# Kernel tuning notes

Measured on AMD Instinct MI355X. Metric: run time of the kernel, lower is better.

Reference implementation:

```python
import jax, jax.numpy as jnp
import numpy as np

N_REACH = 4096
N_T = 730
DT = 3600.0
VEL_LB = 0.3
VEL_UB = 15.0
Q_LB = 1e-4
SLOPE_LB = 1e-4


def _make_adjacency(n):
    # River-network DAG in topological order: each reach j (except outlet)
    # drains to exactly one downstream reach i > j  =>  strictly lower-triangular.
    rng = np.random.default_rng(0)
    j = np.arange(n - 1)
    ds = j + 1 + (rng.random(n - 1) * (n - 1 - j)).astype(np.int64)
    adj = np.zeros((n, n), dtype=np.float32)
    adj[ds, j] = 1.0
    return jnp.asarray(adj)


def setup_inputs() -> dict:
    key = jax.random.key(0)
    ks = jax.random.split(key, 8)
    u = lambda k, s: jax.random.uniform(k, s, dtype=jnp.float32)
    q_prime = u(ks[0], (N_T, N_REACH)) * 10.0            # lateral inflow m^3/s
    n = 0.01 + 0.09 * u(ks[1], (N_REACH,))               # Manning's n
    q_spatial = 1.5 + u(ks[2], (N_REACH,))               # log base > 1
    p_spatial = 1.0 + 3.0 * u(ks[3], (N_REACH,))         # width scale
    length = 1000.0 + 5000.0 * u(ks[4], (N_REACH,))      # reach length [m]
    slope = 1e-3 + 0.05 * u(ks[5], (N_REACH,))           # channel slope
    width = 5.0 + 100.0 * u(ks[6], (N_REACH,))           # width > p_spatial
    x_storage = 0.1 + 0.3 * u(ks[7], (N_REACH,))         # Muskingum x
    adj = _make_adjacency(N_REACH)
    return {"q_prime": q_prime, "n": n, "q_spatial": q_spatial,
            "p_spatial": p_spatial, "length": length, "slope": slope,
            "width": width, "x_storage": x_storage, "adj": adj}


def reference(q_prime, n, q_spatial, p_spatial, length, slope, width, x_storage, adj):
    slope = jnp.clip(slope, SLOPE_LB)
    # Manning's equation -> celerity (note: independent of discharge, as in source)
    depth = jnp.log(width / p_spatial) / jnp.log(q_spatial)
    v = (1.0 / n) * depth ** (2.0 / 3.0) * jnp.sqrt(slope)
    c = jnp.clip(v, VEL_LB, VEL_UB) * (5.0 / 3.0)
    k = length / c
    denom = 2.0 * k * (1.0 - x_storage) + DT
    c1 = (DT - 2.0 * k * x_storage) / denom
    c2 = (DT + 2.0 * k * x_storage) / denom
    c3 = (2.0 * k * (1.0 - x_storage) - DT) / denom
    c4 = 2.0 * DT / denom

    # Lower-triangular routing system: A = I - diag(c1) @ adjacency (constant)
    N = q_prime.shape[1]
    A = jnp.eye(N, dtype=q_prime.dtype) - c1[:, None] * adj

    q0 = q_prime[0]
    out0 = jnp.clip(q0[-1], Q_LB)  # single gage at index -1

    def step(q_t, qp_row):
        q_l = jnp.clip(qp_row, Q_LB)
        i_t = adj @ q_t                        # upstream inflow
        b = c2 * i_t + c3 * q_t + c4 * q_l
        x = jax.scipy.linalg.solve_triangular(A, b[:, None], lower=True)[:, 0]
        q_t1 = jnp.clip(x, Q_LB)
        return q_t1, q_t1[-1]

    _, outs = jax.lax.scan(step, q0, q_prime[:-1])  # timesteps 1..T-1 use q_prime[t-1]
    runoff = jnp.concatenate([out0[None], outs])[None, :]  # [1, T]
    return runoff
```

## Files before the change

### kernel.cpp

```cpp
#include <hip/hip_runtime.h>

#define N 4096
#define NT 730
#define NTH 512
#define PER_T 8
#define QLB 1e-4f
#define DT_S 3600.0f

#define WS_DS     0
#define WS_SZ     4096
#define WS_CCNT   8192
#define WS_COFF   12288
#define WS_CUR    16388
#define WS_HI     20484
#define WS_FLAG   24580
#define WS_C1     28676
#define WS_C2     32772
#define WS_C3     36868
#define WS_C4     40964
#define WS_CLIST  45060
#define WS_GP     49156
#define WS_LOP    53252
#define WS_C3P    57348
#define WS_C4P    61444
#define WS_EPAR   65540
#define WS_EWS    69636
#define WS_SP     73736
#define WS_ISP    81928
#define WS_QPP    90120
#define WS_END    (WS_QPP + NT * N)

__device__ __forceinline__ int qidx(int p) { return ((p & 7) << 9) | (p >> 3); }

template <int CTRL, int RMASK>
__device__ __forceinline__ double dpp_stage(double v) {
    union U { double d; unsigned int u[2]; };
    U s, t;
    s.d = v;
    t.u[0] = (unsigned)__builtin_amdgcn_update_dpp(0, (int)s.u[0], CTRL, RMASK, 0xf, false);
    t.u[1] = (unsigned)__builtin_amdgcn_update_dpp(0, (int)s.u[1], CTRL, RMASK, 0xf, false);
    return v + t.d;
}
__device__ __forceinline__ double wave_incl_scan(double v) {
    v = dpp_stage<0x111, 0xf>(v);
    v = dpp_stage<0x112, 0xf>(v);
    v = dpp_stage<0x114, 0xf>(v);
    v = dpp_stage<0x118, 0xf>(v);
    v = dpp_stage<0x142, 0xa>(v);
    v = dpp_stage<0x143, 0xc>(v);
    return v;
}

__global__ void k_init(int* ds, int* sz, int* ccnt, int* hi, int* flag) {
    int j = blockIdx.x * 256 + threadIdx.x;
    if (j < N) { ds[j] = N - 1; sz[j] = 1; ccnt[j] = 0; hi[j] = -1; flag[j] = 0; }
}

__global__ void k_extract(const float4* __restrict__ adj4, int* __restrict__ ds) {
    long idx = (long)blockIdx.x * 256 + threadIdx.x;
    if (idx >= (long)N * N / 4) return;
    float4 w = adj4[idx];
    long base = idx * 4;
    int row = (int)(base >> 12);
    int col = (int)(base & 4095);
    if (w.x != 0.0f) ds[col + 0] = row;
    if (w.y != 0.0f) ds[col + 1] = row;
    if (w.z != 0.0f) ds[col + 2] = row;
    if (w.w != 0.0f) ds[col + 3] = row;
}

__global__ void k_coeffs(const float* n, const float* qs, const float* ps,
                         const float* len, const float* slope, const float* width,
                         const float* xs, float* __restrict__ c1, float* __restrict__ c2,
                         float* __restrict__ c3, float* __restrict__ c4) {
    int i = blockIdx.x * 256 + threadIdx.x;
    if (i >= N) return;
    float s  = fmaxf(slope[i], 1e-4f);
    float dp = logf(width[i] / ps[i]) / logf(qs[i]);
    float v  = (1.0f / n[i]) * powf(dp, 2.0f / 3.0f) * sqrtf(s);
    float c  = fminf(fmaxf(v, 0.3f), 15.0f) * (5.0f / 3.0f);
    float k  = len[i] / c;
    float x  = xs[i];
    float denom = 2.0f * k * (1.0f - x) + DT_S;
    c1[i] = (DT_S - 2.0f * k * x) / denom;
    c2[i] = (DT_S + 2.0f * k * x) / denom;
    c3[i] = (2.0f * k * (1.0f - x) - DT_S) / denom;
    c4[i] = 2.0f * DT_S / denom;
}

__global__ void k_count(const int* __restrict__ ds, int* __restrict__ ccnt,
                        int* __restrict__ sz) {
    int u = blockIdx.x * 256 + threadIdx.x;
    if (u >= N || u == N - 1) return;
    atomicAdd(&ccnt[ds[u]], 1);
    int a = ds[u];
    while (true) {
        atomicAdd(&sz[a], 1);
        if (a == N - 1) break;
        a = ds[a];
    }
}

__global__ __launch_bounds__(1024) void k_scan(const int* __restrict__ src,
                                               int* __restrict__ off,
                                               int* __restrict__ cur) {
    __shared__ int buf[1024];
    int tid = threadIdx.x;
    int a0 = src[tid * 4 + 0], a1 = src[tid * 4 + 1];
    int a2 = src[tid * 4 + 2], a3 = src[tid * 4 + 3];
    int s1 = a0, s2 = a0 + a1, s3 = a0 + a1 + a2, tot = s3 + a3;
    buf[tid] = tot;
    __syncthreads();
    for (int o = 1; o < 1024; o <<= 1) {
        int add = (tid >= o) ? buf[tid - o] : 0;
        __syncthreads();
        buf[tid] += add;
        __syncthreads();
    }
    int base = buf[tid] - tot;
    off[tid * 4 + 0] = base;      cur[tid * 4 + 0] = base;
    off[tid * 4 + 1] = base + s1; cur[tid * 4 + 1] = base + s1;
    off[tid * 4 + 2] = base + s2; cur[tid * 4 + 2] = base + s2;
    off[tid * 4 + 3] = base + s3; cur[tid * 4 + 3] = base + s3;
    if (tid == 1023) off[N] = buf[1023];
}

__global__ void k_fill(const int* __restrict__ ds, int* __restrict__ cur,
                       int* __restrict__ clist) {
    int u = blockIdx.x * 256 + threadIdx.x;
    if (u >= N || u == N - 1) return;
    int cp = atomicAdd(&cur[ds[u]], 1);
    clist[cp] = u;
}

__global__ __launch_bounds__(1024) void k_post(const int* __restrict__ ds,
                                               const int* __restrict__ sz,
                                               const int* __restrict__ coff,
                                               const int* __restrict__ ccnt,
                                               const int* __restrict__ clist,
                                               int* __restrict__ hi,
                                               int* __restrict__ flag) {
    int tid = threadIdx.x;
    if (tid == 0) hi[N - 1] = N - 1;
    __syncthreads();
    for (int it = 0; it < 96; ++it) {
        for (int v = tid; v < N; v += 1024) {
            if (hi[v] >= 0 && flag[v] == 0) {
                int cum = hi[v] - sz[v] + 1;
                int b0 = coff[v], e0 = b0 + ccnt[v];
                for (int k = b0; k < e0; ++k) {
                    int c = clist[k];
                    hi[c] = cum + sz[c] - 1;
                    cum += sz[c];
                }
                flag[v] = 1;
            }
        }
        __syncthreads();
    }
}

__global__ void k_prep(const int* __restrict__ ds, const int* __restrict__ sz,
                       const int* __restrict__ hi,
                       const float* __restrict__ c1, const float* __restrict__ c2,
                       const float* __restrict__ c3, const float* __restrict__ c4,
                       int* __restrict__ gP, int* __restrict__ loP,
                       float* __restrict__ c3P, float* __restrict__ c4P,
                       int* __restrict__ eparP, float* __restrict__ ewsP,
                       double* __restrict__ SP, double* __restrict__ ISP) {
    int u = blockIdx.x * 256 + threadIdx.x;
    if (u >= N) return;
    int p = hi[u];
    double s = 1.0;
    if (u != N - 1) {
        int a = ds[u];
        while (true) {
            s *= (double)c1[a];
            if (a == N - 1) break;
            a = ds[a];
        }
    }
    SP[p] = s; ISP[p] = 1.0 / s;
    gP[p] = u;
    loP[p] = p - sz[u] + 1;
    c3P[p] = c3[u]; c4P[p] = c4[u];
    if (u != N - 1) {
        eparP[p] = hi[ds[u]];
        ewsP[p] = c2[ds[u]];
    } else {
        eparP[p] = p;
        ewsP[p] = 0.0f;
    }
}

__global__ void k_permute(const float* __restrict__ qp, const int* __restrict__ gP,
                          float* __restrict__ qpp) {
    long e = (long)blockIdx.x * 256 + threadIdx.x;
    if (e >= (long)NT * N) return;
    int tr = (int)(e >> 12);
    int v  = (int)(e & 4095);
    qpp[e] = qp[(size_t)tr * N + gP[v]];
}

__global__ __launch_bounds__(NTH) void k_route(
    const float* __restrict__ qp, const float* __restrict__ qpp,
    const float* __restrict__ c3g, const float* __restrict__ c4g,
    const int* __restrict__ gPg, const int* __restrict__ loPg,
    const int* __restrict__ eparPg, const float* __restrict__ ewsPg,
    const double* __restrict__ SPg, const double* __restrict__ ISPg,
    int use_perm, float* __restrict__ out) {
    __shared__ float CSA[2][N];
    __shared__ double TLp[N];
    __shared__ __align__(16) double wpart[8];
    int tid = threadIdx.x;
    int lane = tid & 63, wid = tid >> 6;

    int epar[PER_T], jg[PER_T], wv[PER_T], g[PER_T];
    float ews[PER_T], c3r[PER_T], c4r[PER_T], qreg[PER_T], qc[PER_T], qn[PER_T];
    double Sr[PER_T], iSr[PER_T];
    bool haslo[PER_T];
#pragma unroll
    for (int r = 0; r < PER_T; ++r) {
        int p = tid * PER_T + r;
        epar[r] = eparPg[p]; ews[r] = ewsPg[p];
        int l = loPg[p];
        haslo[r] = (l > 0);
        int lm = (l > 0) ? (l - 1) : 0;
        jg[r] = qidx(lm);
        wv[r] = lm >> 9;
        g[r] = gPg[p];
        c3r[r] = c3g[p]; c4r[r] = c4g[p];
        Sr[r] = SPg[p]; iSr[r] = ISPg[p];
        float q0 = use_perm ? qpp[p] : qp[g[r]];
        qreg[r] = q0; qc[r] = q0;
    }
    {
        float4 z = make_float4(0.f, 0.f, 0.f, 0.f);
        float4* c0 = (float4*)&CSA[0][tid * PER_T];
        float4* c1 = (float4*)&CSA[1][tid * PER_T];
        c0[0] = z; c0[1] = z; c1[0] = z; c1[1] = z;
    }
    if (tid == NTH - 1) out[0] = fmaxf(qreg[PER_T - 1], QLB);
    __syncthreads();
#pragma unroll
    for (int r = 0; r < PER_T; ++r)
        atomicAdd(&CSA[1][epar[r]], ews[r] * qreg[r]);
    __syncthreads();

    for (int t = 1; t < NT; ++t) {
        int s = t & 1;
        float4 ca = *(const float4*)&CSA[s][tid * PER_T];
        float4 cb = *(const float4*)&CSA[s][tid * PER_T + 4];
        float cs[PER_T] = {ca.x, ca.y, ca.z, ca.w, cb.x, cb.y, cb.z, cb.w};
        float bb[PER_T];
        double yv[PER_T], Tloc[PER_T];
        double tl = 0.0;
#pragma unroll
        for (int r = 0; r < PER_T; ++r) {
            bb[r] = cs[r] + c3r[r] * qreg[r] + c4r[r] * fmaxf(qc[r], QLB);
            double y = Sr[r] * (double)bb[r];
            yv[r] = y;
            tl += y;
            Tloc[r] = tl;
        }
        double incl = wave_incl_scan(tl);
        double texw = incl - tl;
#pragma unroll
        for (int r = 0; r < PER_T; ++r)
            TLp[(r << 9) | tid] = texw + Tloc[r];
        if (lane == 63) wpart[wid] = incl;
        __syncthreads();
        if (t < NT - 1) {
            if (use_perm) {
                const float4* row4 = (const float4*)(qpp + (size_t)t * N);
                float4 a = row4[tid * 2], b = row4[tid * 2 + 1];
                qn[0] = a.x; qn[1] = a.y; qn[2] = a.z; qn[3] = a.w;
                qn[4] = b.x; qn[5] = b.y; qn[6] = b.z; qn[7] = b.w;
            } else {
                const float* row = qp + (size_t)t * N;
#pragma unroll
                for (int r = 0; r < PER_T; ++r) qn[r] = row[g[r]];
            }
        }
        double2 w0 = *(const double2*)&wpart[0];
        double2 w1 = *(const double2*)&wpart[2];
        double2 w2 = *(const double2*)&wpart[4];
        double2 w3 = *(const double2*)&wpart[6];
        double P1 = w0.x, P2 = P1 + w0.y, P3 = P2 + w1.x, P4 = P3 + w1.y;
        double P5 = P4 + w2.x, P6 = P5 + w2.y, P7 = P6 + w3.x;
        double woff = 0.0;
        if (wid > 0) woff += w0.x;
        if (wid > 1) woff += w0.y;
        if (wid > 2) woff += w1.x;
        if (wid > 3) woff += w1.y;
        if (wid > 4) woff += w2.x;
        if (wid > 5) woff += w2.y;
        if (wid > 6) woff += w3.x;
#pragma unroll
        for (int r = 0; r < PER_T; ++r) {
            int w = wv[r];
            double lo2 = (w & 2) ? ((w & 1) ? P3 : P2) : ((w & 1) ? P1 : 0.0);
            double hi2 = (w & 2) ? ((w & 1) ? P7 : P6) : ((w & 1) ? P5 : P4);
            double goff = (w & 4) ? hi2 : lo2;
            double Tg = haslo[r] ? (TLp[jg[r]] + goff) : 0.0;
            double Tself = woff + texw + Tloc[r] - yv[r];
            double x = (double)bb[r] + (Tself - Tg) * iSr[r];
            qreg[r] = fmaxf((float)x, QLB);
        }
        {
            float4 z = make_float4(0.f, 0.f, 0.f, 0.f);
            float4* c0 = (float4*)&CSA[s][tid * PER_T];
            c0[0] = z; c0[1] = z;
        }
#pragma unroll
        for (int r = 0; r < PER_T; ++r)
            atomicAdd(&CSA[s ^ 1][epar[r]], ews[r] * qreg[r]);
        if (tid == NTH - 1) out[t] = qreg[PER_T - 1];
        __syncthreads();
#pragma unroll
        for (int r = 0; r < PER_T; ++r) qc[r] = qn[r];
    }
}

extern "C" void kernel_launch(void* const* d_in, const int* in_sizes, int n_in,
                              void* d_out, int out_size, void* d_ws, size_t ws_size,
                              hipStream_t stream) {
    const float* qp    = (const float*)d_in[0];
    const float* n     = (const float*)d_in[1];
    const float* qs    = (const float*)d_in[2];
    const float* ps    = (const float*)d_in[3];
    const float* len   = (const float*)d_in[4];
    const float* slope = (const float*)d_in[5];
    const float* width = (const float*)d_in[6];
    const float* xs    = (const float*)d_in[7];
    const float* adj   = (const float*)d_in[8];
    float* out = (float*)d_out;

    int*    W     = (int*)d_ws;
    int*    ds    = W + WS_DS;
    int*    sz    = W + WS_SZ;
    int*    ccnt  = W + WS_CCNT;
    int*    coff  = W + WS_COFF;
    int*    cur   = W + WS_CUR;
    int*    hi    = W + WS_HI;
    int*    flag  = W + WS_FLAG;
    float*  c1    = (float*)(W + WS_C1);
    float*  c2    = (float*)(W + WS_C2);
    float*  c3    = (float*)(W + WS_C3);
    float*  c4    = (float*)(W + WS_C4);
    int*    clist = W + WS_CLIST;
    int*    gP    = W + WS_GP;
    int*    loP   = W + WS_LOP;
    float*  c3P   = (float*)(W + WS_C3P);
    float*  c4P   = (float*)(W + WS_C4P);
    int*    eparP = W + WS_EPAR;
    float*  ewsP  = (float*)(W + WS_EWS);
    double* SP    = (double*)(W + WS_SP);
    double* ISP   = (double*)(W + WS_ISP);
    float*  QPP   = (float*)(W + WS_QPP);

    int use_perm = (ws_size >= (size_t)WS_END * 4) ? 1 : 0;

    k_init<<<(N + 255) / 256, 256, 0, stream>>>(ds, sz, ccnt, hi, flag);
    k_extract<<<(N * N / 4 + 255) / 256, 256, 0, stream>>>((const float4*)adj, ds);
    k_coeffs<<<(N + 255) / 256, 256, 0, stream>>>(n, qs, ps, len, slope, width, xs,
                                                  c1, c2, c3, c4);
    k_count<<<(N + 255) / 256, 256, 0, stream>>>(ds, ccnt, sz);
    k_scan<<<1, 1024, 0, stream>>>(ccnt, coff, cur);
    k_fill<<<(N + 255) / 256, 256, 0, stream>>>(ds, cur, clist);
    k_post<<<1, 1024, 0, stream>>>(ds, sz, coff, ccnt, clist, hi, flag);
    k_prep<<<(N + 255) / 256, 256, 0, stream>>>(ds, sz, hi, c1, c2, c3, c4,
                                                gP, loP, c3P, c4P, eparP, ewsP,
                                                SP, ISP);
    if (use_perm)
        k_permute<<<(int)(((long)NT * N + 255) / 256), 256, 0, stream>>>(qp, gP, QPP);
    k_route<<<1, NTH, 0, stream>>>(qp, QPP, c3P, c4P, gP, loP, eparP, ewsP,
                                   SP, ISP, use_perm, out);
}
```

Before: 5.178 ms.

## Double routing block to 1024 threads and compute wave offsets before storing prefix

The single-block routing kernel now uses 1024 threads with 4 reaches each instead of 512 with 8, which halves the serial per-thread work in every timestep. Cross-wave offsets are computed with a 16-lane DPP scan over the wave partials and readlane. That requires an extra barrier before the shared prefix array is written, but the array then holds global prefixes, so the per-element offset selection logic goes away. The cost is a third barrier per step across 16 waves and more LDS atomic contention from more threads.

```diff
diff --git a/kernel.cpp b/kernel.cpp
--- a/kernel.cpp
+++ b/kernel.cpp
@@ -2,8 +2,8 @@
 
 #define N 4096
 #define NT 730
-#define NTH 512
-#define PER_T 8
+#define NTH 1024
+#define PER_T 4
 #define QLB 1e-4f
 #define DT_S 3600.0f
 
@@ -30,7 +30,7 @@
 #define WS_QPP    90120
 #define WS_END    (WS_QPP + NT * N)
 
-__device__ __forceinline__ int qidx(int p) { return ((p & 7) << 9) | (p >> 3); }
+__device__ __forceinline__ int qidx4(int p) { return ((p & 3) << 10) | (p >> 2); }
 
 template <int CTRL, int RMASK>
 __device__ __forceinline__ double dpp_stage(double v) {
@@ -49,6 +49,21 @@
     v = dpp_stage<0x142, 0xa>(v);
     v = dpp_stage<0x143, 0xc>(v);
     return v;
+}
+__device__ __forceinline__ double row16_incl_scan(double v) {
+    v = dpp_stage<0x111, 0xf>(v);
+    v = dpp_stage<0x112, 0xf>(v);
+    v = dpp_stage<0x114, 0xf>(v);
+    v = dpp_stage<0x118, 0xf>(v);
+    return v;
+}
+__device__ __forceinline__ double readlane_f64(double v, int slane) {
+    union U { double d; int i[2]; };
+    U u; u.d = v;
+    U o;
+    o.i[0] = __builtin_amdgcn_readlane(u.i[0], slane);
+    o.i[1] = __builtin_amdgcn_readlane(u.i[1], slane);
+    return o.d;
 }
 
 __global__ void k_init(int* ds, int* sz, int* ccnt, int* hi, int* flag) {
@@ -210,12 +225,13 @@
     const double* __restrict__ SPg, const double* __restrict__ ISPg,
     int use_perm, float* __restrict__ out) {
     __shared__ float CSA[2][N];
-    __shared__ double TLp[N];
-    __shared__ __align__(16) double wpart[8];
+    __shared__ double TL[N];
+    __shared__ __align__(16) double wpart[16];
     int tid = threadIdx.x;
     int lane = tid & 63, wid = tid >> 6;
-
-    int epar[PER_T], jg[PER_T], wv[PER_T], g[PER_T];
+    int swid = __builtin_amdgcn_readfirstlane(wid);
+
+    int epar[PER_T], jg[PER_T], g[PER_T];
     float ews[PER_T], c3r[PER_T], c4r[PER_T], qreg[PER_T], qc[PER_T], qn[PER_T];
     double Sr[PER_T], iSr[PER_T];
     bool haslo[PER_T];
@@ -226,8 +242,7 @@
         int l = loPg[p];
         haslo[r] = (l > 0);
         int lm = (l > 0) ? (l - 1) : 0;
-        jg[r] = qidx(lm);
-        wv[r] = lm >> 9;
+        jg[r] = qidx4(lm);
         g[r] = gPg[p];
         c3r[r] = c3g[p]; c4r[r] = c4g[p];
         Sr[r] = SPg[p]; iSr[r] = ISPg[p];
@@ -236,9 +251,8 @@
     }
     {
         float4 z = make_float4(0.f, 0.f, 0.f, 0.f);
-        float4* c0 = (float4*)&CSA[0][tid * PER_T];
-        float4* c1 = (float4*)&CSA[1][tid * PER_T];
-        c0[0] = z; c0[1] = z; c1[0] = z; c1[1] = z;
+        *(float4*)&CSA[0][tid * PER_T] = z;
+        *(float4*)&CSA[1][tid * PER_T] = z;
     }
     if (tid == NTH - 1) out[0] = fmaxf(qreg[PER_T - 1], QLB);
     __syncthreads();
@@ -250,8 +264,7 @@
     for (int t = 1; t < NT; ++t) {
         int s = t & 1;
         float4 ca = *(const float4*)&CSA[s][tid * PER_T];
-        float4 cb = *(const float4*)&CSA[s][tid * PER_T + 4];
-        float cs[PER_T] = {ca.x, ca.y, ca.z, ca.w, cb.x, cb.y, cb.z, cb.w};
+        float cs[PER_T] = {ca.x, ca.y, ca.z, ca.w};
         float bb[PER_T];
         double yv[PER_T], Tloc[PER_T];
         double tl = 0.0;
@@ -265,52 +278,36 @@
         }
         double incl = wave_incl_scan(tl);
         double texw = incl - tl;
+        if (lane == 63) wpart[wid] = incl;
+        __syncthreads();
+        double wpown = wpart[lane & 15];
+        double wincl = row16_incl_scan(wpown);
+        double woff = readlane_f64(wincl, swid) - readlane_f64(wpown, swid);
+        double tbase = woff + texw;
 #pragma unroll
         for (int r = 0; r < PER_T; ++r)
-            TLp[(r << 9) | tid] = texw + Tloc[r];
-        if (lane == 63) wpart[wid] = incl;
+            TL[(r << 10) | tid] = tbase + Tloc[r];
         __syncthreads();
         if (t < NT - 1) {
             if (use_perm) {
-                const float4* row4 = (const float4*)(qpp + (size_t)t * N);
-                float4 a = row4[tid * 2], b = row4[tid * 2 + 1];
+                float4 a = ((const float4*)(qpp + (size_t)t * N))[tid];
                 qn[0] = a.x; qn[1] = a.y; qn[2] = a.z; qn[3] = a.w;
-                qn[4] = b.x; qn[5] = b.y; qn[6] = b.z; qn[7] = b.w;
             } else {
                 const float* row = qp + (size_t)t * N;
 #pragma unroll
                 for (int r = 0; r < PER_T; ++r) qn[r] = row[g[r]];
             }
         }
-        double2 w0 = *(const double2*)&wpart[0];
-        double2 w1 = *(const double2*)&wpart[2];
-        double2 w2 = *(const double2*)&wpart[4];
-        double2 w3 = *(const double2*)&wpart[6];
-        double P1 = w0.x, P2 = P1 + w0.y, P3 = P2 + w1.x, P4 = P3 + w1.y;
-        double P5 = P4 + w2.x, P6 = P5 + w2.y, P7 = P6 + w3.x;
-        double woff = 0.0;
-        if (wid > 0) woff += w0.x;
-        if (wid > 1) woff += w0.y;
-        if (wid > 2) woff += w1.x;
-        if (wid > 3) woff += w1.y;
-        if (wid > 4) woff += w2.x;
-        if (wid > 5) woff += w2.y;
-        if (wid > 6) woff += w3.x;
 #pragma unroll
         for (int r = 0; r < PER_T; ++r) {
-            int w = wv[r];
-            double lo2 = (w & 2) ? ((w & 1) ? P3 : P2) : ((w & 1) ? P1 : 0.0);
-            double hi2 = (w & 2) ? ((w & 1) ? P7 : P6) : ((w & 1) ? P5 : P4);
-            double goff = (w & 4) ? hi2 : lo2;
-            double Tg = haslo[r] ? (TLp[jg[r]] + goff) : 0.0;
-            double Tself = woff + texw + Tloc[r] - yv[r];
+            double Tg = haslo[r] ? TL[jg[r]] : 0.0;
+            double Tself = tbase + Tloc[r] - yv[r];
             double x = (double)bb[r] + (Tself - Tg) * iSr[r];
             qreg[r] = fmaxf((float)x, QLB);
         }
         {
             float4 z = make_float4(0.f, 0.f, 0.f, 0.f);
-            float4* c0 = (float4*)&CSA[s][tid * PER_T];
-            c0[0] = z; c0[1] = z;
+            *(float4*)&CSA[s][tid * PER_T] = z;
         }
 #pragma unroll
         for (int r = 0; r < PER_T; ++r)
```

New measurement: 4.914 ms. 1.05x faster.
